# Performance work log

Hardware: AMD Instinct MI355X
Metric: run time of the kernel (lower is better)

Reference implementation:

```python
import jax, jax.numpy as jnp
import numpy as np

N = 8192          # num nodes
F_DIM = 32        # input feature dim
E_DIM = 32        # embedding_dim
SUPPORT = 4       # num relations
NUM_BASES = 2     # basis decomposition size


def setup_inputs() -> dict:
    key = jax.random.key(0)
    k1, k2, k3, k4 = jax.random.split(key, 4)
    features = jax.random.normal(k1, (N, F_DIM), dtype=jnp.float32)
    A = jax.random.normal(k2, (SUPPORT, N, N), dtype=jnp.float32)
    W = jax.random.normal(k3, (NUM_BASES, F_DIM, E_DIM), dtype=jnp.float32) * 0.05
    W_comp = jax.random.normal(k4, (SUPPORT, NUM_BASES), dtype=jnp.float32) * 0.05
    return {"features": features, "A": A, "W": W, "W_comp": W_comp}


def reference(features, A, W, W_comp):
    # Per-relation aggregation: supports[s] = A[s] @ features  -> [S, N, F]
    supports = jnp.einsum('snm,mf->snf', A, features)
    # Concatenate along axis=1 (feature axis): column order is s-major (s*F + f)
    n = features.shape[0]
    supports_ = jnp.transpose(supports, (1, 0, 2)).reshape(n, SUPPORT * F_DIM)
    # Basis decomposition, exactly as original:
    # W: (B, F, E) -> transpose (F, B, E); V = W_comp @ W -> (F, S, E)
    Wt = jnp.transpose(W, (1, 0, 2))                       # [F, B, E]
    V = jnp.einsum('sb,fbe->fse', W_comp, Wt)              # [F, S, E]
    V = V.reshape(SUPPORT * F_DIM, E_DIM)                  # row order f-major (f*S + s), faithful to original
    return supports_ @ V                                   # [N, E]
```

## Files before the change

### kernel.cpp

```cpp
#include <hip/hip_runtime.h>

#define NND 8192
#define FD  32
#define ED  32
#define SUP 4
#define NB  2

#define TM  64
#define TMP 68
#define KSPLIT 8

__global__ __launch_bounds__(256) void prep_g(
        const float* __restrict__ features,
        const float* __restrict__ W,
        const float* __restrict__ Wc,
        float* __restrict__ G,
        float* __restrict__ out) {
    __shared__ __align__(16) float Vlds[SUP * FD * ED];
    const int t = threadIdx.x;

    for (int i = t; i < SUP * FD * ED; i += 256) {
        const int e  = i & 31;
        const int f  = (i >> 5) & 31;
        const int s  = i >> 10;
        const int f2 = s * 8 + (f >> 2);
        const int s2 = f & 3;
        float v = 0.f;
        #pragma unroll
        for (int b = 0; b < NB; ++b)
            v += Wc[s2 * NB + b] * W[(b * FD + f2) * ED + e];
        Vlds[i] = v;
    }
    __syncthreads();

    const int gid = blockIdx.x * 256 + t;
    if (gid < NND * ED) out[gid] = 0.f;

    const float4* feat4 = (const float4*)features;
    #pragma unroll
    for (int i = 0; i < 4; ++i) {
        const int o = gid + i * (1024 * 256);
        const int e = o & 31;
        const int m = (o >> 5) & (NND - 1);
        const int s = o >> 18;
        float acc = 0.f;
        #pragma unroll
        for (int f4 = 0; f4 < 8; ++f4) {
            const float4 fv = feat4[m * 8 + f4];
            acc += fv.x * Vlds[s * 1024 + (f4 * 4 + 0) * 32 + e];
            acc += fv.y * Vlds[s * 1024 + (f4 * 4 + 1) * 32 + e];
            acc += fv.z * Vlds[s * 1024 + (f4 * 4 + 2) * 32 + e];
            acc += fv.w * Vlds[s * 1024 + (f4 * 4 + 3) * 32 + e];
        }
        G[o] = acc;
    }
}

#define FMA4(acc, sa, g) { acc.x += (sa) * (g).x; acc.y += (sa) * (g).y; \
                           acc.z += (sa) * (g).z; acc.w += (sa) * (g).w; }

__global__ __launch_bounds__(256) void rgcn_main(
        const float* __restrict__ A,
        const float* __restrict__ G,
        float* __restrict__ out) {
    __shared__ __align__(16) float Asb[128 * TMP];
    __shared__ __align__(16) float Gsb[TM * 32];

    const int t  = threadIdx.x;
    const int bx = blockIdx.x;
    const int nb = bx & 63;
    const int kb = bx >> 6;
    const int s       = kb >> 1;
    const int m_start = (kb & 1) * 4096;
    const int n0      = nb * 128;

    const float* Abase = A + ((size_t)s * NND + n0) * NND;
    const float* Gbase = G + (size_t)s * NND * 32;

    const int eg = t & 7;
    const int r  = t >> 3;

    float4 acc0 = {0.f, 0.f, 0.f, 0.f};
    float4 acc1 = acc0, acc2 = acc0, acc3 = acc0;

    for (int step = 0; step < 4096 / TM; ++step) {
        const int m0 = m_start + step * TM;
        __syncthreads();
        #pragma unroll
        for (int it = 0; it < 8; ++it) {
            const int q   = it * 256 + t;
            const int row = q >> 4;
            const int c4  = q & 15;
            const float4 v = *(const float4*)(Abase + (size_t)row * NND + m0 + c4 * 4);
            *(float4*)&Asb[row * TMP + c4 * 4] = v;
        }
        const float4* gsrc = (const float4*)(Gbase + (size_t)m0 * 32);
        #pragma unroll
        for (int it = 0; it < 2; ++it) {
            const int q = it * 256 + t;
            ((float4*)Gsb)[q] = gsrc[q];
        }
        __syncthreads();

        #pragma unroll
        for (int k4 = 0; k4 < TM; k4 += 4) {
            const float4 a0 = *(const float4*)&Asb[(r +  0) * TMP + k4];
            const float4 a1 = *(const float4*)&Asb[(r + 32) * TMP + k4];
            const float4 a2 = *(const float4*)&Asb[(r + 64) * TMP + k4];
            const float4 a3 = *(const float4*)&Asb[(r + 96) * TMP + k4];
            const float4 g0 = *(const float4*)&Gsb[(k4 + 0) * 32 + eg * 4];
            const float4 g1 = *(const float4*)&Gsb[(k4 + 1) * 32 + eg * 4];
            const float4 g2 = *(const float4*)&Gsb[(k4 + 2) * 32 + eg * 4];
            const float4 g3 = *(const float4*)&Gsb[(k4 + 3) * 32 + eg * 4];

            FMA4(acc0, a0.x, g0); FMA4(acc0, a0.y, g1); FMA4(acc0, a0.z, g2); FMA4(acc0, a0.w, g3);
            FMA4(acc1, a1.x, g0); FMA4(acc1, a1.y, g1); FMA4(acc1, a1.z, g2); FMA4(acc1, a1.w, g3);
            FMA4(acc2, a2.x, g0); FMA4(acc2, a2.y, g1); FMA4(acc2, a2.z, g2); FMA4(acc2, a2.w, g3);
            FMA4(acc3, a3.x, g0); FMA4(acc3, a3.y, g1); FMA4(acc3, a3.z, g2); FMA4(acc3, a3.w, g3);
        }
    }

    #pragma unroll
    for (int j = 0; j < 4; ++j) {
        const float4 a = (j == 0) ? acc0 : (j == 1) ? acc1 : (j == 2) ? acc2 : acc3;
        float* p = out + (size_t)(n0 + r + 32 * j) * 32 + eg * 4;
        atomicAdd(p + 0, a.x);
        atomicAdd(p + 1, a.y);
        atomicAdd(p + 2, a.z);
        atomicAdd(p + 3, a.w);
    }
}

extern "C" void kernel_launch(void* const* d_in, const int* in_sizes, int n_in,
                              void* d_out, int out_size, void* d_ws, size_t ws_size,
                              hipStream_t stream) {
    const float* features = (const float*)d_in[0];
    const float* A        = (const float*)d_in[1];
    const float* W        = (const float*)d_in[2];
    const float* Wc       = (const float*)d_in[3];
    float* out = (float*)d_out;
    float* G   = (float*)d_ws;

    prep_g<<<1024, 256, 0, stream>>>(features, W, Wc, G, out);
    rgcn_main<<<64 * KSPLIT, 256, 0, stream>>>(A, G, out);
}
```

Before: 1.414 ms.

## Double-buffer A/G tiles via direct global-to-LDS loads with larger register tiles

```diff
diff --git a/kernel.cpp b/kernel.cpp
--- a/kernel.cpp
+++ b/kernel.cpp
@@ -6,9 +6,17 @@
 #define SUP 4
 #define NB  2
 
-#define TM  64
-#define TMP 68
-#define KSPLIT 8
+#define BROWS 256
+#define TK    32
+#define CHUNK 2048
+#define NSTEP (CHUNK/TK)
+
+#define FMA4(acc, sa, g) { acc.x += (sa) * (g).x; acc.y += (sa) * (g).y; \
+                           acc.z += (sa) * (g).z; acc.w += (sa) * (g).w; }
+
+#define GLDS16(gsrc, ldst) \
+  __builtin_amdgcn_global_load_lds((const __attribute__((address_space(1))) void*)(gsrc), \
+                                   (__attribute__((address_space(3))) void*)(ldst), 16, 0, 0)
 
 __global__ __launch_bounds__(256) void prep_g(
         const float* __restrict__ features,
@@ -16,13 +24,15 @@
         const float* __restrict__ Wc,
         float* __restrict__ G,
         float* __restrict__ out) {
-    __shared__ __align__(16) float Vlds[SUP * FD * ED];
-    const int t = threadIdx.x;
+    __shared__ __align__(16) float Vlds[FD * ED];
+    const int t   = threadIdx.x;
+    const int gid = blockIdx.x * 256 + t;
+    const int s   = gid >> 13;
+    const int m   = gid & (NND - 1);
 
-    for (int i = t; i < SUP * FD * ED; i += 256) {
+    for (int i = t; i < FD * ED; i += 256) {
         const int e  = i & 31;
-        const int f  = (i >> 5) & 31;
-        const int s  = i >> 10;
+        const int f  = i >> 5;
         const int f2 = s * 8 + (f >> 2);
         const int s2 = f & 3;
         float v = 0.f;
@@ -33,101 +43,130 @@
     }
     __syncthreads();
 
-    const int gid = blockIdx.x * 256 + t;
-    if (gid < NND * ED) out[gid] = 0.f;
+    float4* out4 = (float4*)out;
+    const float4 z = {0.f, 0.f, 0.f, 0.f};
+    out4[gid]         = z;
+    out4[gid + 32768] = z;
 
-    const float4* feat4 = (const float4*)features;
+    const float4* feat4 = (const float4*)(features + (size_t)m * FD);
+    float4 fr[8];
     #pragma unroll
-    for (int i = 0; i < 4; ++i) {
-        const int o = gid + i * (1024 * 256);
-        const int e = o & 31;
-        const int m = (o >> 5) & (NND - 1);
-        const int s = o >> 18;
-        float acc = 0.f;
+    for (int i = 0; i < 8; ++i) fr[i] = feat4[i];
+
+    float4 acc[8];
+    #pragma unroll
+    for (int i = 0; i < 8; ++i) acc[i] = z;
+
+    const float4* V4 = (const float4*)Vlds;
+    #pragma unroll
+    for (int f = 0; f < FD; ++f) {
+        const float fv = ((const float*)fr)[f];
         #pragma unroll
-        for (int f4 = 0; f4 < 8; ++f4) {
-            const float4 fv = feat4[m * 8 + f4];
-            acc += fv.x * Vlds[s * 1024 + (f4 * 4 + 0) * 32 + e];
-            acc += fv.y * Vlds[s * 1024 + (f4 * 4 + 1) * 32 + e];
-            acc += fv.z * Vlds[s * 1024 + (f4 * 4 + 2) * 32 + e];
-            acc += fv.w * Vlds[s * 1024 + (f4 * 4 + 3) * 32 + e];
+        for (int e4 = 0; e4 < 8; ++e4) {
+            const float4 v = V4[f * 8 + e4];
+            FMA4(acc[e4], fv, v);
         }
-        G[o] = acc;
     }
+    float4* g4 = (float4*)(G + ((size_t)s * NND + m) * ED);
+    #pragma unroll
+    for (int e4 = 0; e4 < 8; ++e4) g4[e4] = acc[e4];
 }
 
-#define FMA4(acc, sa, g) { acc.x += (sa) * (g).x; acc.y += (sa) * (g).y; \
-                           acc.z += (sa) * (g).z; acc.w += (sa) * (g).w; }
-
-__global__ __launch_bounds__(256) void rgcn_main(
+__global__ __launch_bounds__(128, 1) void rgcn_main(
         const float* __restrict__ A,
         const float* __restrict__ G,
         float* __restrict__ out) {
-    __shared__ __align__(16) float Asb[128 * TMP];
-    __shared__ __align__(16) float Gsb[TM * 32];
+    __shared__ __align__(16) float Asb[2][BROWS * TK];
+    __shared__ __align__(16) float Gsb[2][TK * ED];
 
     const int t  = threadIdx.x;
     const int bx = blockIdx.x;
-    const int nb = bx & 63;
-    const int kb = bx >> 6;
-    const int s       = kb >> 1;
-    const int m_start = (kb & 1) * 4096;
-    const int n0      = nb * 128;
+    const int nb = bx & 31;
+    const int kb = bx >> 5;
+    const int s       = kb >> 2;
+    const int m_start = (kb & 3) * CHUNK;
+    const int n0      = nb * BROWS;
 
-    const float* Abase = A + ((size_t)s * NND + n0) * NND;
-    const float* Gbase = G + (size_t)s * NND * 32;
+    const float* Ab = A + ((size_t)s * NND + n0) * NND + m_start;
+    const float* Gb = G + (size_t)s * NND * ED + (size_t)m_start * ED;
 
-    const int eg = t & 7;
-    const int r  = t >> 3;
+    const int w    = t >> 6;
+    const int lane = t & 63;
+    const int lr   = lane >> 3;
+    const int lc   = lane & 7;
 
-    float4 acc0 = {0.f, 0.f, 0.f, 0.f};
-    float4 acc1 = acc0, acc2 = acc0, acc3 = acc0;
+    auto stage = [&](int step, int buf) {
+        const int m0 = step * TK;
+        #pragma unroll
+        for (int i = 0; i < 16; ++i) {
+            const int inst = w * 16 + i;
+            const int row  = inst * 8 + lr;
+            const int c4   = lc ^ (inst & 7);
+            GLDS16(Ab + (size_t)row * NND + m0 + (c4 << 2), &Asb[buf][inst * 256]);
+        }
+        #pragma unroll
+        for (int i = 0; i < 2; ++i) {
+            const int inst = w * 2 + i;
+            GLDS16(Gb + (size_t)m0 * ED + inst * 256 + lane * 4, &Gsb[buf][inst * 256]);
+        }
+    };
 
-    for (int step = 0; step < 4096 / TM; ++step) {
-        const int m0 = m_start + step * TM;
-        __syncthreads();
+    const int rg = t >> 2;
+    const int eg = t & 3;
+    const int sw = rg & 7;
+
+    float4 acc[8][2];
+    #pragma unroll
+    for (int i = 0; i < 8; ++i) {
+        acc[i][0] = float4{0.f, 0.f, 0.f, 0.f};
+        acc[i][1] = float4{0.f, 0.f, 0.f, 0.f};
+    }
+
+    stage(0, 0);
+    __syncthreads();
+
+    for (int step = 0; step < NSTEP; ++step) {
+        const int buf = step & 1;
+        if (step + 1 < NSTEP) stage(step + 1, buf ^ 1);
+
+        const float* As = Asb[buf];
+        const float* Gs = Gsb[buf];
         #pragma unroll
-        for (int it = 0; it < 8; ++it) {
-            const int q   = it * 256 + t;
-            const int row = q >> 4;
-            const int c4  = q & 15;
-            const float4 v = *(const float4*)(Abase + (size_t)row * NND + m0 + c4 * 4);
-            *(float4*)&Asb[row * TMP + c4 * 4] = v;
-        }
-        const float4* gsrc = (const float4*)(Gbase + (size_t)m0 * 32);
-        #pragma unroll
-        for (int it = 0; it < 2; ++it) {
-            const int q = it * 256 + t;
-            ((float4*)Gsb)[q] = gsrc[q];
+        for (int k4 = 0; k4 < 8; ++k4) {
+            float4 a[8];
+            #pragma unroll
+            for (int i = 0; i < 8; ++i)
+                a[i] = *(const float4*)&As[(rg * 8 + i) * TK + ((k4 ^ sw) << 2)];
+            float4 g[4][2];
+            #pragma unroll
+            for (int kk = 0; kk < 4; ++kk) {
+                g[kk][0] = *(const float4*)&Gs[(k4 * 4 + kk) * ED + eg * 8];
+                g[kk][1] = *(const float4*)&Gs[(k4 * 4 + kk) * ED + eg * 8 + 4];
+            }
+            #pragma unroll
+            for (int i = 0; i < 8; ++i) {
+                #pragma unroll
+                for (int h = 0; h < 2; ++h) {
+                    FMA4(acc[i][h], a[i].x, g[0][h]);
+                    FMA4(acc[i][h], a[i].y, g[1][h]);
+                    FMA4(acc[i][h], a[i].z, g[2][h]);
+                    FMA4(acc[i][h], a[i].w, g[3][h]);
+                }
+            }
         }
         __syncthreads();
-
-        #pragma unroll
-        for (int k4 = 0; k4 < TM; k4 += 4) {
-            const float4 a0 = *(const float4*)&Asb[(r +  0) * TMP + k4];
-            const float4 a1 = *(const float4*)&Asb[(r + 32) * TMP + k4];
-            const float4 a2 = *(const float4*)&Asb[(r + 64) * TMP + k4];
-            const float4 a3 = *(const float4*)&Asb[(r + 96) * TMP + k4];
-            const float4 g0 = *(const float4*)&Gsb[(k4 + 0) * 32 + eg * 4];
-            const float4 g1 = *(const float4*)&Gsb[(k4 + 1) * 32 + eg * 4];
-            const float4 g2 = *(const float4*)&Gsb[(k4 + 2) * 32 + eg * 4];
-            const float4 g3 = *(const float4*)&Gsb[(k4 + 3) * 32 + eg * 4];
-
-            FMA4(acc0, a0.x, g0); FMA4(acc0, a0.y, g1); FMA4(acc0, a0.z, g2); FMA4(acc0, a0.w, g3);
-            FMA4(acc1, a1.x, g0); FMA4(acc1, a1.y, g1); FMA4(acc1, a1.z, g2); FMA4(acc1, a1.w, g3);
-            FMA4(acc2, a2.x, g0); FMA4(acc2, a2.y, g1); FMA4(acc2, a2.z, g2); FMA4(acc2, a2.w, g3);
-            FMA4(acc3, a3.x, g0); FMA4(acc3, a3.y, g1); FMA4(acc3, a3.z, g2); FMA4(acc3, a3.w, g3);
-        }
     }
 
     #pragma unroll
-    for (int j = 0; j < 4; ++j) {
-        const float4 a = (j == 0) ? acc0 : (j == 1) ? acc1 : (j == 2) ? acc2 : acc3;
-        float* p = out + (size_t)(n0 + r + 32 * j) * 32 + eg * 4;
-        atomicAdd(p + 0, a.x);
-        atomicAdd(p + 1, a.y);
-        atomicAdd(p + 2, a.z);
-        atomicAdd(p + 3, a.w);
+    for (int i = 0; i < 8; ++i) {
+        float* p = out + (size_t)(n0 + rg * 8 + i) * ED + eg * 8;
+        #pragma unroll
+        for (int h = 0; h < 2; ++h) {
+            atomicAdd(p + h * 4 + 0, acc[i][h].x);
+            atomicAdd(p + h * 4 + 1, acc[i][h].y);
+            atomicAdd(p + h * 4 + 2, acc[i][h].z);
+            atomicAdd(p + h * 4 + 3, acc[i][h].w);
+        }
     }
 }
 
@@ -141,6 +180,6 @@
     float* out = (float*)d_out;
     float* G   = (float*)d_ws;
 
-    prep_g<<<1024, 256, 0, stream>>>(features, W, Wc, G, out);
-    rgcn_main<<<64 * KSPLIT, 256, 0, stream>>>(A, G, out);
+    prep_g<<<128, 256, 0, stream>>>(features, W, Wc, G, out);
+    rgcn_main<<<32 * 16, 128, 0, stream>>>(A, G, out);
 }
```

Result: slower. 1.551 ms (+9.7%).
